# Optimization experiments

Hardware: AMD Instinct MI355X
Metric: run time of the kernel (lower is better)

Reference implementation:

```python
import jax, jax.numpy as jnp
import numpy as np

N = 100000      # number of nodes
E = 1600000     # number of (directed) edges, avg degree 16
DIN = 128       # in_features
DOUT = 32       # out_features
SLOPE = 0.2     # leaky relu negative slope


def setup_inputs() -> dict:
    key = jax.random.key(0)
    k1, k2, k3, k4, k5, k6 = jax.random.split(key, 6)
    x = jax.random.normal(k1, (N, DIN), dtype=jnp.float32)
    edge_index = jax.random.randint(k2, (2, E), 0, N, dtype=jnp.int32)
    # W1 (shared with W2 and used as the feature-update matrix W, 'source' mode)
    W1_w = jax.random.normal(k3, (DOUT, DIN), dtype=jnp.float32) / np.float32(np.sqrt(DIN))
    W1_b = jax.random.normal(k4, (DOUT,), dtype=jnp.float32) * 0.01
    a1_w = jax.random.normal(k5, (DOUT,), dtype=jnp.float32) / np.float32(np.sqrt(DOUT))
    a2_w = jax.random.normal(k6, (DOUT,), dtype=jnp.float32) / np.float32(np.sqrt(DOUT))
    return {"x": x, "edge_index": edge_index, "W1_w": W1_w, "W1_b": W1_b,
            "a1_w": a1_w, "a2_w": a2_w}


def reference(x, edge_index, W1_w, W1_b, a1_w, a2_w):
    n = x.shape[0]
    # append self-loops, as in _sparse_attention
    loops = jnp.arange(n, dtype=edge_index.dtype)
    src = jnp.concatenate([edge_index[0], loops])   # rows  (softmax segments)
    dst = jnp.concatenate([edge_index[1], loops])   # cols
    # h = W1(x) (linear, with bias); W2 = W1 (weight sharing), W = W2 ('source')
    h = x @ W1_w.T + W1_b                           # [N, DOUT]
    z = jax.nn.leaky_relu(h, SLOPE)                 # x1 == x2 under weight sharing
    s1 = z @ a1_w                                   # [N] per-node src score
    s2 = z @ a2_w                                   # [N] per-node dst score
    logits = s1[src] + s2[dst]                      # [E+N] per-edge attention logit
    # row-wise (dim=1) sparse softmax == segment softmax over src
    m = jax.ops.segment_max(logits, src, num_segments=n)
    ex = jnp.exp(logits - m[src])
    denom = jax.ops.segment_sum(ex, src, num_segments=n)
    alpha = ex / denom[src]                         # normalized attention per edge
    # sparse-dense matmul: out[i] = sum_{(i,j)} alpha_ij * h[j]
    return jax.ops.segment_sum(alpha[:, None] * h[dst], src, num_segments=n)
```

## Files before the change

kernel.cpp:

```cpp
#include <hip/hip_runtime.h>
#include <hip/hip_fp16.h>

#define DIN 128
#define DOUT 32
#define SLOPE 0.2f

#define BSHIFT 7
#define BNODES 128
#define NBS    1024
#define CAP    3072
#define SRTCAP (CAP + 384)
#define TILE   4096
#define EPB    (TILE / 256)

#define FSMEM  16384

typedef short s16x8 __attribute__((ext_vector_type(8)));
typedef float f32x4 __attribute__((ext_vector_type(4)));

__device__ __forceinline__ short f2bf(float f) {
    unsigned u = __float_as_uint(f);
    return (short)((u + 0x7fffu + ((u >> 16) & 1u)) >> 16);
}
__device__ __forceinline__ float bf2f(short s) {
    return __uint_as_float(((unsigned)(unsigned short)s) << 16);
}

__device__ __forceinline__ void linear_tile(
    int tile, int ntiles, int lane, int N,
    const unsigned short* __restrict__ Whi, const unsigned short* __restrict__ Wlo,
    const float* __restrict__ x,
    const float* __restrict__ b, const float* __restrict__ a2,
    __half* __restrict__ g16, float* __restrict__ es2)
{
    if (tile >= ntiles) return;
    int m = lane & 15, oct = lane >> 4;

    s16x8 bh[2][4], bl[2][4];
    #pragma unroll
    for (int t = 0; t < 2; ++t) {
        int row = t * 16 + m;
        #pragma unroll
        for (int kc = 0; kc < 4; ++kc) {
            int sch = (kc * 4 + oct) ^ m;
            bh[t][kc] = *(const s16x8*)((const char*)Whi + row * 256 + sch * 16);
            bl[t][kc] = *(const s16x8*)((const char*)Wlo + row * 256 + sch * 16);
        }
    }

    int c0 = m, c1 = 16 + m;
    float b0 = b[c0], b1 = b[c1], A0 = a2[c0], A1 = a2[c1];

    long rowbase = (long)tile * 16;
    long lrow = rowbase + m; if (lrow > N - 1) lrow = N - 1;
    const float* xrow = x + lrow * DIN + oct * 8;
    f32x4 acc0 = {0.f, 0.f, 0.f, 0.f}, acc1 = {0.f, 0.f, 0.f, 0.f};
    #pragma unroll
    for (int kc = 0; kc < 4; ++kc) {
        float4 x0 = *(const float4*)(xrow + kc * 32);
        float4 x1 = *(const float4*)(xrow + kc * 32 + 4);
        float xf[8] = {x0.x, x0.y, x0.z, x0.w, x1.x, x1.y, x1.z, x1.w};
        s16x8 ah, al;
        #pragma unroll
        for (int j = 0; j < 8; ++j) {
            short hh = f2bf(xf[j]);
            ah[j] = hh;
            al[j] = f2bf(xf[j] - bf2f(hh));
        }
        acc0 = __builtin_amdgcn_mfma_f32_16x16x32_bf16(al, bh[0][kc], acc0, 0, 0, 0);
        acc0 = __builtin_amdgcn_mfma_f32_16x16x32_bf16(ah, bl[0][kc], acc0, 0, 0, 0);
        acc0 = __builtin_amdgcn_mfma_f32_16x16x32_bf16(ah, bh[0][kc], acc0, 0, 0, 0);
        acc1 = __builtin_amdgcn_mfma_f32_16x16x32_bf16(al, bh[1][kc], acc1, 0, 0, 0);
        acc1 = __builtin_amdgcn_mfma_f32_16x16x32_bf16(ah, bl[1][kc], acc1, 0, 0, 0);
        acc1 = __builtin_amdgcn_mfma_f32_16x16x32_bf16(ah, bh[1][kc], acc1, 0, 0, 0);
    }

    float hv0[4], hv1[4], sp[4];
    #pragma unroll
    for (int i = 0; i < 4; ++i) {
        hv0[i] = acc0[i] + b0;
        hv1[i] = acc1[i] + b1;
        float z0 = hv0[i] > 0.f ? hv0[i] : SLOPE * hv0[i];
        float z1 = hv1[i] > 0.f ? hv1[i] : SLOPE * hv1[i];
        sp[i] = z0 * A0 + z1 * A1;
    }
    #pragma unroll
    for (int off = 1; off <= 8; off <<= 1) {
        #pragma unroll
        for (int i = 0; i < 4; ++i) sp[i] += __shfl_xor(sp[i], off, 64);
    }
    #pragma unroll
    for (int i = 0; i < 4; ++i) {
        long r = rowbase + oct * 4 + i;
        if (r >= N) continue;
        float ev = __expf(sp[i]);
        g16[r * DOUT + c0] = __float2half(ev * hv0[i]);
        g16[r * DOUT + c1] = __float2half(ev * hv1[i]);
        if (m == 0) es2[r] = ev;
    }
}

__global__ __launch_bounds__(256) void gat_fused(
    const float* __restrict__ x, const float* __restrict__ W,
    const float* __restrict__ b, const float* __restrict__ a2,
    const int* __restrict__ src, const int* __restrict__ dst,
    __half* __restrict__ g16, float* __restrict__ es2,
    unsigned* __restrict__ ebuf, int* __restrict__ boffT,
    int N, int E, int ntiles, int nbin, int nbinp)
{
    __shared__ __align__(16) unsigned char smem[FSMEM];
    int tid = threadIdx.x;

    if ((int)blockIdx.x >= nbin) {
        unsigned short* Whi = (unsigned short*)smem;
        unsigned short* Wlo = (unsigned short*)(smem + 8192);
        for (int c = tid; c < 512; c += 256) {
            int row = c >> 4, ch = c & 15;
            const float* wsrc = W + (long)row * DIN + ch * 8;
            float4 a  = *(const float4*)wsrc;
            float4 b4 = *(const float4*)(wsrc + 4);
            float wf[8] = {a.x, a.y, a.z, a.w, b4.x, b4.y, b4.z, b4.w};
            s16x8 hi, lo;
            #pragma unroll
            for (int j = 0; j < 8; ++j) {
                short hh = f2bf(wf[j]);
                hi[j] = hh;
                lo[j] = f2bf(wf[j] - bf2f(hh));
            }
            int sch = ch ^ (row & 15);
            *(s16x8*)((char*)Whi + row * 256 + sch * 16) = hi;
            *(s16x8*)((char*)Wlo + row * 256 + sch * 16) = lo;
        }
        __syncthreads();
        int wave = tid >> 6;
        int tile = ((int)blockIdx.x - nbin) * 4 + wave;
        linear_tile(tile, ntiles, tid & 63, N, Whi, Wlo, x, b, a2, g16, es2);
        return;
    }

    int* cnt   = (int*)smem;
    int* offs  = (int*)(smem + 4096);
    int* wsum  = (int*)(smem + 8192);
    int* wbase = (int*)(smem + 8208);
    long tstart = (long)blockIdx.x * TILE;

    for (int i = tid; i < NBS; i += 256) cnt[i] = 0;
    __syncthreads();

    unsigned rec[EPB];
    int      bq[EPB];
    #pragma unroll
    for (int it = 0; it < EPB; ++it) {
        long e = tstart + it * 256 + tid;
        int s = (e < E) ? src[e] : -1;
        int d = (e < E) ? dst[e] : 0;
        if (s >= 0) {
            int bk = s >> BSHIFT;
            int rv = atomicAdd(&cnt[bk], 1);
            rec[it] = ((unsigned)(s & (BNODES - 1)) << 17) | (unsigned)d;
            bq[it] = (rv < 511) ? ((bk << 9) | rv) : -1;
        } else bq[it] = -1;
    }
    __syncthreads();

    int t4 = tid << 2;
    int c0 = cnt[t4], c1 = cnt[t4 + 1], c2 = cnt[t4 + 2], c3 = cnt[t4 + 3];
    int s4 = c0 + c1 + c2 + c3;
    int v = s4;
    #pragma unroll
    for (int off = 1; off < 64; off <<= 1) {
        int t = __shfl_up(v, off, 64);
        if ((tid & 63) >= off) v += t;
    }
    if ((tid & 63) == 63) wsum[tid >> 6] = v;
    __syncthreads();
    if (tid == 0) {
        int a = 0;
        #pragma unroll
        for (int w = 0; w < 4; ++w) { wbase[w] = a; a += wsum[w]; }
    }
    __syncthreads();
    int base = wbase[tid >> 6] + (v - s4);
    offs[t4]     = base;
    offs[t4 + 1] = base + c0;
    offs[t4 + 2] = base + c0 + c1;
    offs[t4 + 3] = base + c0 + c1 + c2;
    __syncthreads();

    int NBv = (N + BNODES - 1) >> BSHIFT;
    for (int i = tid; i <= NBv; i += 256)
        boffT[(size_t)i * nbinp + blockIdx.x] = offs[i];

    #pragma unroll
    for (int it = 0; it < EPB; ++it) {
        int q = bq[it];
        if (q >= 0) {
            int pos = offs[q >> 9] + (q & 511);
            ebuf[tstart + pos] = rec[it];
        }
    }
}

__global__ __launch_bounds__(512) void gat_aggregate(
    const __half* __restrict__ g16, const float* __restrict__ es2,
    const unsigned* __restrict__ ebuf, const int* __restrict__ boffT,
    float* __restrict__ out, int N, int nbin, int nbinp)
{
    __shared__ unsigned srt[SRTCAP];
    __shared__ unsigned srca[CAP];
    __shared__ int cnt[BNODES];
    __shared__ int basep[BNODES];
    __shared__ int pos2[BNODES];
    __shared__ int wsum[8], wbase[8], totsh;
    int tid = threadIdx.x;

    int nwg = gridDim.x;
    int xcd = blockIdx.x & 7;
    int q = nwg >> 3, rr = nwg & 7;
    int bk = (xcd < rr ? xcd * (q + 1) : rr * (q + 1) + (xcd - rr) * q)
           + ((int)blockIdx.x >> 3);

    if (tid < BNODES) { cnt[tid] = 0; pos2[tid] = 0; }

    int rstart = 0, rlen = 0;
    if (tid < nbin) {
        rstart = boffT[(size_t)bk * nbinp + tid];
        rlen   = boffT[(size_t)(bk + 1) * nbinp + tid] - rstart;
    }
    int v = rlen;
    #pragma unroll
    for (int off = 1; off < 64; off <<= 1) {
        int t = __shfl_up(v, off, 64);
        if ((tid & 63) >= off) v += t;
    }
    if ((tid & 63) == 63) wsum[tid >> 6] = v;
    __syncthreads();
    if (tid == 0) {
        int a = 0;
        #pragma unroll
        for (int w = 0; w < 8; ++w) { wbase[w] = a; a += wsum[w]; }
        totsh = a;
    }
    __syncthreads();
    int dest = wbase[tid >> 6] + (v - rlen);
    int lim = CAP - dest; if (lim < 0) lim = 0;
    if (rlen > lim) rlen = lim;
    {
        unsigned abase = (unsigned)tid * TILE + (unsigned)rstart;
        for (int j = 0; j < rlen; ++j)
            srca[dest + j] = abase + (unsigned)j;
    }
    __syncthreads();
    int cntb = totsh; if (cntb > CAP) cntb = CAP;

    unsigned held[6];
    #pragma unroll
    for (int k = 0; k < 6; ++k) {
        int r = tid + (k << 9);
        held[k] = 0xFFFFFFFFu;
        if (r < cntb) held[k] = ebuf[(size_t)srca[r]];
    }
    #pragma unroll
    for (int k = 0; k < 6; ++k) {
        unsigned u = held[k];
        if (u != 0xFFFFFFFFu) atomicAdd(&cnt[u >> 17], 1);
    }
    __syncthreads();

    if (tid < 64) {
        int a = cnt[2 * tid], b2 = cnt[2 * tid + 1];
        int pa = (a + 3) & ~3, pb = (b2 + 3) & ~3;
        int s = pa + pb;
        int vv = s;
        #pragma unroll
        for (int off = 1; off < 64; off <<= 1) {
            int t = __shfl_up(vv, off, 64);
            if (tid >= off) vv += t;
        }
        int excl = vv - s;
        basep[2 * tid]     = excl;
        basep[2 * tid + 1] = excl + pa;
    }
    __syncthreads();

    #pragma unroll
    for (int k = 0; k < 6; ++k) {
        unsigned u = held[k];
        if (u != 0xFFFFFFFFu) {
            int sl = (int)(u >> 17);
            int p = basep[sl] + atomicAdd(&pos2[sl], 1);
            srt[p] = u & 0x1FFFFu;
        }
    }
    __syncthreads();

    int unit = tid >> 5, col = tid & 31;
    int lane64 = tid & 63;
    for (int sl = unit; sl < BNODES; sl += 16) {
        long node = (long)bk * BNODES + sl;
        if (node >= N) break;
        float acc = __half2float(g16[node * DOUT + col]);
        float selfe = es2[node];
        float dpart = 0.f;
        int e = basep[sl], e_end = basep[sl] + cnt[sl];

        while (e + 8 <= e_end) {
            uint4 q0 = *(const uint4*)&srt[e];
            uint4 q1 = *(const uint4*)&srt[e + 4];
            float evp = 0.f;
            if (col < 8) evp = es2[srt[e + col]];
            int dn[8] = {(int)q0.x, (int)q0.y, (int)q0.z, (int)q0.w,
                         (int)q1.x, (int)q1.y, (int)q1.z, (int)q1.w};
            unsigned short gv[8];
            #pragma unroll
            for (int j = 0; j < 8; ++j)
                gv[j] = *(const unsigned short*)&g16[(long)dn[j] * DOUT + col];
            dpart += evp;
            #pragma unroll
            for (int j = 0; j < 8; ++j)
                acc += __half2float(*(const __half*)&gv[j]);
            e += 8;
        }
        while (e + 4 <= e_end) {
            uint4 q0 = *(const uint4*)&srt[e];
            float evp = 0.f;
            if (col < 4) evp = es2[srt[e + col]];
            int dn[4] = {(int)q0.x, (int)q0.y, (int)q0.z, (int)q0.w};
            unsigned short gv[4];
            #pragma unroll
            for (int j = 0; j < 4; ++j)
                gv[j] = *(const unsigned short*)&g16[(long)dn[j] * DOUT + col];
            dpart += evp;
            #pragma unroll
            for (int j = 0; j < 4; ++j)
                acc += __half2float(*(const __half*)&gv[j]);
            e += 4;
        }
        for (; e < e_end; ++e) {
            int dn = (int)srt[e];
            acc += __half2float(g16[(long)dn * DOUT + col]);
            if (col == 0) dpart += es2[dn];
        }
        #pragma unroll
        for (int off = 1; off < 8; off <<= 1)
            dpart += __shfl_xor(dpart, off, 64);
        float dtot = __shfl(dpart, lane64 & 32, 64);
        out[node * DOUT + col] = acc / (selfe + dtot);
    }
}

extern "C" void kernel_launch(void* const* d_in, const int* in_sizes, int n_in,
                              void* d_out, int out_size, void* d_ws, size_t ws_size,
                              hipStream_t stream)
{
    const float* x  = (const float*)d_in[0];
    const int*   ei = (const int*)d_in[1];
    const float* W  = (const float*)d_in[2];
    const float* b  = (const float*)d_in[3];
    const float* a2 = (const float*)d_in[5];
    float* out = (float*)d_out;

    int N = in_sizes[0] / DIN;
    int E = in_sizes[1] / 2;
    const int* src = ei;
    const int* dst = ei + E;

    int NB = (N + BNODES - 1) >> BSHIFT;
    int nbin = (E + TILE - 1) / TILE;
    int nbinp = (nbin + 7) & ~7;

    char* ws = (char*)d_ws;
    __half*   g16   = (__half*)ws;  ws += (size_t)N * DOUT * sizeof(__half);
    float*    es2   = (float*)ws;   ws += (size_t)N * sizeof(float);
    int*      boffT = (int*)ws;     ws += (size_t)(NB + 1) * nbinp * sizeof(int);
    unsigned* ebuf  = (unsigned*)ws; ws += (size_t)nbin * TILE * sizeof(unsigned);

    int ntiles = (N + 15) / 16;
    int nlin   = (ntiles + 3) / 4;

    gat_fused    <<<nbin + nlin, 256, 0, stream>>>(x, W, b, a2, src, dst,
                                                   g16, es2, ebuf, boffT,
                                                   N, E, ntiles, nbin, nbinp);
    gat_aggregate<<<NB, 512, 0, stream>>>(g16, es2, ebuf, boffT, out, N,
                                          nbin, nbinp);
}
```

Baseline: 148.8 us.

## Split fp16 feature table into two column halves and gather each half separately

```diff
diff --git a/kernel.cpp b/kernel.cpp
--- a/kernel.cpp
+++ b/kernel.cpp
@@ -31,7 +31,8 @@
     const unsigned short* __restrict__ Whi, const unsigned short* __restrict__ Wlo,
     const float* __restrict__ x,
     const float* __restrict__ b, const float* __restrict__ a2,
-    __half* __restrict__ g16, float* __restrict__ es2)
+    __half* __restrict__ g16a, __half* __restrict__ g16b,
+    float* __restrict__ es2)
 {
     if (tile >= ntiles) return;
     int m = lane & 15, oct = lane >> 4;
@@ -94,8 +95,8 @@
         long r = rowbase + oct * 4 + i;
         if (r >= N) continue;
         float ev = __expf(sp[i]);
-        g16[r * DOUT + c0] = __float2half(ev * hv0[i]);
-        g16[r * DOUT + c1] = __float2half(ev * hv1[i]);
+        g16a[r * 16 + m] = __float2half(ev * hv0[i]);
+        g16b[r * 16 + m] = __float2half(ev * hv1[i]);
         if (m == 0) es2[r] = ev;
     }
 }
@@ -104,7 +105,8 @@
     const float* __restrict__ x, const float* __restrict__ W,
     const float* __restrict__ b, const float* __restrict__ a2,
     const int* __restrict__ src, const int* __restrict__ dst,
-    __half* __restrict__ g16, float* __restrict__ es2,
+    __half* __restrict__ g16a, __half* __restrict__ g16b,
+    float* __restrict__ es2,
     unsigned* __restrict__ ebuf, int* __restrict__ boffT,
     int N, int E, int ntiles, int nbin, int nbinp)
 {
@@ -134,7 +136,8 @@
         __syncthreads();
         int wave = tid >> 6;
         int tile = ((int)blockIdx.x - nbin) * 4 + wave;
-        linear_tile(tile, ntiles, tid & 63, N, Whi, Wlo, x, b, a2, g16, es2);
+        linear_tile(tile, ntiles, tid & 63, N, Whi, Wlo, x, b, a2,
+                    g16a, g16b, es2);
         return;
     }
 
@@ -202,7 +205,8 @@
 }
 
 __global__ __launch_bounds__(512) void gat_aggregate(
-    const __half* __restrict__ g16, const float* __restrict__ es2,
+    const __half* __restrict__ g16a, const __half* __restrict__ g16b,
+    const float* __restrict__ es2,
     const unsigned* __restrict__ ebuf, const int* __restrict__ boffT,
     float* __restrict__ out, int N, int nbin, int nbinp)
 {
@@ -294,58 +298,84 @@
     }
     __syncthreads();
 
-    int unit = tid >> 5, col = tid & 31;
-    int lane64 = tid & 63;
-    for (int sl = unit; sl < BNODES; sl += 16) {
-        long node = (long)bk * BNODES + sl;
-        if (node >= N) break;
-        float acc = __half2float(g16[node * DOUT + col]);
-        float selfe = es2[node];
-        float dpart = 0.f;
-        int e = basep[sl], e_end = basep[sl] + cnt[sl];
-
-        while (e + 8 <= e_end) {
-            uint4 q0 = *(const uint4*)&srt[e];
-            uint4 q1 = *(const uint4*)&srt[e + 4];
-            float evp = 0.f;
-            if (col < 8) evp = es2[srt[e + col]];
-            int dn[8] = {(int)q0.x, (int)q0.y, (int)q0.z, (int)q0.w,
-                         (int)q1.x, (int)q1.y, (int)q1.z, (int)q1.w};
-            unsigned short gv[8];
-            #pragma unroll
-            for (int j = 0; j < 8; ++j)
-                gv[j] = *(const unsigned short*)&g16[(long)dn[j] * DOUT + col];
-            dpart += evp;
-            #pragma unroll
-            for (int j = 0; j < 8; ++j)
-                acc += __half2float(*(const __half*)&gv[j]);
-            e += 8;
-        }
-        while (e + 4 <= e_end) {
-            uint4 q0 = *(const uint4*)&srt[e];
-            float evp = 0.f;
-            if (col < 4) evp = es2[srt[e + col]];
-            int dn[4] = {(int)q0.x, (int)q0.y, (int)q0.z, (int)q0.w};
-            unsigned short gv[4];
-            #pragma unroll
-            for (int j = 0; j < 4; ++j)
-                gv[j] = *(const unsigned short*)&g16[(long)dn[j] * DOUT + col];
-            dpart += evp;
-            #pragma unroll
-            for (int j = 0; j < 4; ++j)
-                acc += __half2float(*(const __half*)&gv[j]);
-            e += 4;
-        }
-        for (; e < e_end; ++e) {
-            int dn = (int)srt[e];
-            acc += __half2float(g16[(long)dn * DOUT + col]);
-            if (col == 0) dpart += es2[dn];
-        }
-        #pragma unroll
-        for (int off = 1; off < 8; off <<= 1)
-            dpart += __shfl_xor(dpart, off, 64);
-        float dtot = __shfl(dpart, lane64 & 32, 64);
-        out[node * DOUT + col] = acc / (selfe + dtot);
+    int unit = tid >> 5;
+    int l32  = tid & 31;
+    int c    = l32 & 15;
+    int eoff = l32 >> 4;
+    float dinv[8];
+    #pragma unroll 1
+    for (int p = 0; p < 2; ++p) {
+        const __half* gp = p ? g16b : g16a;
+        #pragma unroll
+        for (int s = 0; s < 8; ++s) {
+            int sl = unit + (s << 4);
+            long node = (long)bk * BNODES + sl;
+            if (node >= N) continue;
+            float acc = (eoff == 0)
+                      ? __half2float(gp[node * 16 + c]) : 0.f;
+            float dpart = 0.f;
+            int e = basep[sl], e_end = basep[sl] + cnt[sl];
+
+            while (e + 16 <= e_end) {
+                uint4 q0 = *(const uint4*)&srt[e];
+                uint4 q1 = *(const uint4*)&srt[e + 4];
+                uint4 q2 = *(const uint4*)&srt[e + 8];
+                uint4 q3 = *(const uint4*)&srt[e + 12];
+                float evp = (p == 0 && l32 < 16) ? es2[srt[e + l32]] : 0.f;
+                int dn[8];
+                dn[0] = (int)(eoff ? q0.y : q0.x);
+                dn[1] = (int)(eoff ? q0.w : q0.z);
+                dn[2] = (int)(eoff ? q1.y : q1.x);
+                dn[3] = (int)(eoff ? q1.w : q1.z);
+                dn[4] = (int)(eoff ? q2.y : q2.x);
+                dn[5] = (int)(eoff ? q2.w : q2.z);
+                dn[6] = (int)(eoff ? q3.y : q3.x);
+                dn[7] = (int)(eoff ? q3.w : q3.z);
+                unsigned short gv[8];
+                #pragma unroll
+                for (int j = 0; j < 8; ++j)
+                    gv[j] = *(const unsigned short*)&gp[(long)dn[j] * 16 + c];
+                dpart += evp;
+                #pragma unroll
+                for (int j = 0; j < 8; ++j)
+                    acc += __half2float(*(const __half*)&gv[j]);
+                e += 16;
+            }
+            if (e < e_end) {
+                int rem = e_end - e;
+                uint4 q0 = *(const uint4*)&srt[e];
+                uint4 q1 = (rem > 4)  ? *(const uint4*)&srt[e + 4]  : q0;
+                uint4 q2 = (rem > 8)  ? *(const uint4*)&srt[e + 8]  : q0;
+                uint4 q3 = (rem > 12) ? *(const uint4*)&srt[e + 12] : q0;
+                float evp = (p == 0 && l32 < 16 && e + l32 < e_end)
+                          ? es2[srt[e + l32]] : 0.f;
+                int dn[8];
+                dn[0] = (int)(eoff ? q0.y : q0.x);
+                dn[1] = (int)(eoff ? q0.w : q0.z);
+                dn[2] = (int)(eoff ? q1.y : q1.x);
+                dn[3] = (int)(eoff ? q1.w : q1.z);
+                dn[4] = (int)(eoff ? q2.y : q2.x);
+                dn[5] = (int)(eoff ? q2.w : q2.z);
+                dn[6] = (int)(eoff ? q3.y : q3.x);
+                dn[7] = (int)(eoff ? q3.w : q3.z);
+                dpart += evp;
+                #pragma unroll
+                for (int j = 0; j < 8; ++j) {
+                    int idx = 2 * j + eoff;
+                    if (idx < rem)
+                        acc += __half2float(gp[(long)dn[j] * 16 + c]);
+                }
+            }
+            if (p == 0) {
+                #pragma unroll
+                for (int off = 1; off <= 16; off <<= 1)
+                    dpart += __shfl_xor(dpart, off, 64);
+                dinv[s] = 1.f / (es2[node] + dpart);
+            }
+            acc += __shfl_xor(acc, 16, 64);
+            if (eoff == 0)
+                out[node * DOUT + (p << 4) + c] = acc * dinv[s];
+        }
     }
 }
 
@@ -370,7 +400,8 @@
     int nbinp = (nbin + 7) & ~7;
 
     char* ws = (char*)d_ws;
-    __half*   g16   = (__half*)ws;  ws += (size_t)N * DOUT * sizeof(__half);
+    __half*   g16a  = (__half*)ws;  ws += (size_t)N * 16 * sizeof(__half);
+    __half*   g16b  = (__half*)ws;  ws += (size_t)N * 16 * sizeof(__half);
     float*    es2   = (float*)ws;   ws += (size_t)N * sizeof(float);
     int*      boffT = (int*)ws;     ws += (size_t)(NB + 1) * nbinp * sizeof(int);
     unsigned* ebuf  = (unsigned*)ws; ws += (size_t)nbin * TILE * sizeof(unsigned);
@@ -379,8 +410,8 @@
     int nlin   = (ntiles + 3) / 4;
 
     gat_fused    <<<nbin + nlin, 256, 0, stream>>>(x, W, b, a2, src, dst,
-                                                   g16, es2, ebuf, boffT,
+                                                   g16a, g16b, es2, ebuf, boffT,
                                                    N, E, ntiles, nbin, nbinp);
-    gat_aggregate<<<NB, 512, 0, stream>>>(g16, es2, ebuf, boffT, out, N,
+    gat_aggregate<<<NB, 512, 0, stream>>>(g16a, g16b, es2, ebuf, boffT, out, N,
                                           nbin, nbinp);
 }
```

Measured after the change: 213.9 us. +43.7%, slower.
